# Kernel optimization log

Hardware: AMD Instinct MI355X
Metric: run time of the kernel (lower is better)

Reference implementation:

```python
import jax, jax.numpy as jnp
from jax import lax
import numpy as np

N, T, F, H, L, TOPK = 2048, 64, 16, 64, 16, 10


def setup_inputs() -> dict:
    key = jax.random.key(0)
    ks = jax.random.split(key, 12)
    s_ih = 1.0 / np.sqrt(H)
    inp = {
        "x": jax.random.normal(ks[0], (N, T, F), dtype=jnp.float32),
        # GRU params (torch layout: weight_ih_l0 (3H,F), weight_hh_l0 (3H,H))
        "W_ih": jax.random.uniform(ks[1], (3 * H, F), minval=-s_ih, maxval=s_ih),
        "W_hh": jax.random.uniform(ks[2], (3 * H, H), minval=-s_ih, maxval=s_ih),
        "b_ih": jax.random.uniform(ks[3], (3 * H,), minval=-s_ih, maxval=s_ih),
        "b_hh": jax.random.uniform(ks[4], (3 * H,), minval=-s_ih, maxval=s_ih),
        "Wq": jax.random.normal(ks[5], (H, H)) * (1.0 / np.sqrt(H)),
        "Wk": jax.random.normal(ks[6], (H, H)) * (1.0 / np.sqrt(H)),
        "W1": jax.random.normal(ks[7], (F, F)) * (1.0 / np.sqrt(F)),
        "b1": jnp.zeros((F,), jnp.float32),
        "W2": jax.random.normal(ks[8], (1, F)) * (1.0 / np.sqrt(F)),
        "b2": jnp.zeros((1,), jnp.float32),
    }
    return inp


def _gru(x, W_ih, W_hh, b_ih, b_hh):
    # x: (N, T, F) -> hidden states (N, T, H)
    xp = x @ W_ih.T + b_ih  # precompute input gates: (N, T, 3H)

    def step(h, xt):
        gh = h @ W_hh.T + b_hh
        xr, xz, xn = jnp.split(xt, 3, axis=-1)
        hr, hz, hn = jnp.split(gh, 3, axis=-1)
        r = jax.nn.sigmoid(xr + hr)
        z = jax.nn.sigmoid(xz + hz)
        n = jnp.tanh(xn + r * hn)
        h_new = (1.0 - z) * n + z * h
        return h_new, h_new

    h0 = jnp.zeros((x.shape[0], W_hh.shape[1]), x.dtype)
    _, hs = lax.scan(step, h0, jnp.swapaxes(xp, 0, 1))  # (T, N, H)
    return jnp.swapaxes(hs, 0, 1)


def reference(x, W_ih, W_hh, b_ih, b_hh, Wq, Wk, W1, b1, W2, b2):
    n, t, f = x.shape
    h = _gru(x, W_ih, W_hh, b_ih, b_hh)          # (N, T, H)
    queries = h[:, -1, :] @ Wq.T                 # (N, H)
    keys = h[:, -L:, :] @ Wk.T                   # (N, L, H)
    # cross-sample scores: query i vs key (stock m, lag l)
    scores = jnp.einsum("nh,mlh->nml", queries, keys)  # (N, N, L)
    eye = jnp.eye(n, dtype=bool)[:, :, None]
    scores = jnp.where(eye, jnp.float32(-1e9), scores)
    flat = scores.reshape(n, n * L)
    topk_vals, topk_idx = lax.top_k(flat, TOPK)  # order differs from torch sorted=False but math is permutation-invariant
    leader_idx = topk_idx // L                   # (N, k)
    lag_idx = topk_idx % L
    time_idx = t - (L - lag_idx)
    leader_feats = x[leader_idx, time_idx]       # (N, k, F)
    w = jax.nn.softmax(topk_vals, axis=1)
    weighted = jnp.sum(leader_feats * w[..., None], axis=1)  # (N, F)
    hid = jax.nn.leaky_relu(weighted @ W1.T + b1, negative_slope=0.01)
    out = (hid @ W2.T + b2).reshape(-1)          # (N,)
    return out
```

## Files before the change

### kernel.cpp

```cpp
#include <hip/hip_runtime.h>

#define NN 2048
#define TT 64
#define FF 16
#define HH 64
#define LL 16
#define TOPKK 10
#define CAP 960

#define AS 72
#define XAS 40
#define XPS 196

typedef __bf16 bf16x8 __attribute__((ext_vector_type(8)));
typedef float floatx4 __attribute__((ext_vector_type(4)));

union FragCast { uint4 u; bf16x8 b; unsigned short s[8]; };

__device__ __forceinline__ unsigned short f2bf(float f) {
    unsigned u = __float_as_uint(f);
    return (unsigned short)((u + 0x7fff + ((u >> 16) & 1)) >> 16);
}
__device__ __forceinline__ float bf2f(unsigned short h) {
    return __uint_as_float(((unsigned)h) << 16);
}
__device__ __forceinline__ void split3(float v, unsigned short& a, unsigned short& b, unsigned short& c) {
    a = f2bf(v); float r = v - bf2f(a);
    b = f2bf(r); float r2 = r - bf2f(b);
    c = f2bf(r2);
}
__device__ __forceinline__ float fsigmoid(float x) {
    return __builtin_amdgcn_rcpf(1.f + __builtin_amdgcn_exp2f(-1.442695041f * x));
}
__device__ __forceinline__ float ftanh(float x) {
    return 1.f - 2.f * __builtin_amdgcn_rcpf(1.f + __builtin_amdgcn_exp2f(2.885390082f * x));
}
__device__ __forceinline__ void async_copy16(const void* g, void* l) {
    __builtin_amdgcn_global_load_lds(
        (const __attribute__((address_space(1))) unsigned int*)g,
        (__attribute__((address_space(3))) unsigned int*)l, 16, 0, 0);
}
#define MFMA16(A, B, C) __builtin_amdgcn_mfma_f32_16x16x32_bf16((A), (B), (C), 0, 0, 0)
#define LIMB6(ACC, A1, A2, A3, W)            \
    ACC = MFMA16((A1), (W)[0], ACC);         \
    ACC = MFMA16((A1), (W)[1], ACC);         \
    ACC = MFMA16((A2), (W)[0], ACC);         \
    ACC = MFMA16((A1), (W)[2], ACC);         \
    ACC = MFMA16((A2), (W)[1], ACC);         \
    ACC = MFMA16((A3), (W)[0], ACC);

__global__ __launch_bounds__(256, 2) void gru_kernel(
    const float* __restrict__ x,
    const float* __restrict__ W_ih,
    const float* __restrict__ W_hh,
    const float* __restrict__ b_ih,
    const float* __restrict__ b_hh,
    float* __restrict__ h_tail)
{
    __shared__ __attribute__((aligned(16))) unsigned short Asp[2][3][16 * AS];
    __shared__ __attribute__((aligned(16))) unsigned short xa[3][16 * XAS];
    __shared__ __attribute__((aligned(16))) float xp[16 * XPS];
    __shared__ __attribute__((aligned(16))) float x_lds[4 * TT * FF];

    const int t    = threadIdx.x;
    const int wv   = t >> 6;
    const int lane = t & 63;
    const int nh   = lane & 15;
    const int quad = lane >> 4;
    const int n0   = blockIdx.x * 4;

    {
        const char* src = (const char*)(x + (size_t)n0 * TT * FF);
        char* dst = (char*)x_lds;
#pragma unroll
        for (int i = 0; i < 4; ++i)
            async_copy16(src + i * 4096 + t * 16, dst + i * 4096 + t * 16);
    }
    {
        unsigned* p = (unsigned*)&Asp[0][0][0];
        for (int i = t; i < 2 * 3 * 16 * AS / 2; i += 256) p[i] = 0;
        unsigned* q = (unsigned*)&xa[0][0];
        for (int i = t; i < 3 * 16 * XAS / 2; i += 256) q[i] = 0;
    }

    const int jb = wv * 16 + nh;
    const float brz = b_ih[jb] + b_hh[jb];
    const float bz  = b_ih[64 + jb] + b_hh[64 + jb];
    const float bxn = b_ih[128 + jb];
    const float bhn = b_hh[128 + jb];

    bf16x8 wf[3][2][3];
#pragma unroll
    for (int nt = 0; nt < 3; ++nt) {
        const int gr = (wv + 4 * nt) * 16 + nh;
#pragma unroll
        for (int kc = 0; kc < 2; ++kc) {
            const float* p = W_hh + gr * 64 + kc * 32 + quad * 8;
            FragCast f1, f2, f3;
#pragma unroll
            for (int i = 0; i < 8; ++i) split3(p[i], f1.s[i], f2.s[i], f3.s[i]);
            wf[nt][kc][0] = f1.b; wf[nt][kc][1] = f2.b; wf[nt][kc][2] = f3.b;
        }
    }
    bf16x8 wfi[3][3];
#pragma unroll
    for (int nt = 0; nt < 3; ++nt) {
        const int gr = (wv + 4 * nt) * 16 + nh;
        FragCast f1, f2, f3;
#pragma unroll
        for (int i = 0; i < 8; ++i) {
            const float v = (quad < 2) ? W_ih[gr * 16 + quad * 8 + i] : 0.f;
            split3(v, f1.s[i], f2.s[i], f3.s[i]);
        }
        wfi[nt][0] = f1.b; wfi[nt][1] = f2.b; wfi[nt][2] = f3.b;
    }

    __syncthreads();

    float hprev = 0.f;

    for (int chunk = 0; chunk < 16; ++chunk) {
        {
            const int row = t >> 4, f = t & 15;
            const int p = row & 3, sl = row >> 2;
            const float xv = x_lds[p * (TT * FF) + (chunk * 4 + sl) * FF + f];
            unsigned short a, b, c; split3(xv, a, b, c);
            xa[0][row * XAS + f] = a;
            xa[1][row * XAS + f] = b;
            xa[2][row * XAS + f] = c;
        }
        __syncthreads();
        {
            floatx4 xacc0 = {0.f,0.f,0.f,0.f}, xacc1 = {0.f,0.f,0.f,0.f}, xacc2 = {0.f,0.f,0.f,0.f};
            const int aoff = nh * XAS + quad * 8;
            FragCast a1, a2, a3;
            a1.u = *(const uint4*)&xa[0][aoff];
            a2.u = *(const uint4*)&xa[1][aoff];
            a3.u = *(const uint4*)&xa[2][aoff];
            LIMB6(xacc0, a1.b, a2.b, a3.b, wfi[0]);
            LIMB6(xacc1, a1.b, a2.b, a3.b, wfi[1]);
            LIMB6(xacc2, a1.b, a2.b, a3.b, wfi[2]);
#pragma unroll
            for (int r = 0; r < 4; ++r) {
                const int m = quad * 4 + r;
                xp[m * XPS + (wv + 0) * 16 + nh] = xacc0[r];
                xp[m * XPS + (wv + 4) * 16 + nh] = xacc1[r];
                xp[m * XPS + (wv + 8) * 16 + nh] = xacc2[r];
            }
        }
        __syncthreads();

#pragma unroll
        for (int si = 0; si < 4; ++si) {
            const int step = chunk * 4 + si;
            const int rb = step & 1, wb = rb ^ 1;
            floatx4 acc0 = {0.f,0.f,0.f,0.f}, acc1 = {0.f,0.f,0.f,0.f}, acc2 = {0.f,0.f,0.f,0.f};
#pragma unroll
            for (int kc = 0; kc < 2; ++kc) {
                const int aoff = nh * AS + kc * 32 + quad * 8;
                FragCast a1, a2, a3;
                a1.u = *(const uint4*)&Asp[rb][0][aoff];
                a2.u = *(const uint4*)&Asp[rb][1][aoff];
                a3.u = *(const uint4*)&Asp[rb][2][aoff];
                LIMB6(acc0, a1.b, a2.b, a3.b, wf[0][kc]);
                LIMB6(acc1, a1.b, a2.b, a3.b, wf[1][kc]);
                LIMB6(acc2, a1.b, a2.b, a3.b, wf[2][kc]);
            }
            {
                const int xrow = si * 4 + quad;
                const float xr = xp[xrow * XPS + jb];
                const float xz = xp[xrow * XPS + 64 + jb];
                const float xn = xp[xrow * XPS + 128 + jb];
                const float rg = fsigmoid(acc0[0] + xr + brz);
                const float zg = fsigmoid(acc1[0] + xz + bz);
                const float ng = ftanh((xn + bxn) + rg * (acc2[0] + bhn));
                const float h  = (1.f - zg) * ng + zg * hprev;
                hprev = h;
                unsigned short la, lb2, lc; split3(h, la, lb2, lc);
                const int ho = (4 * quad) * AS + jb;
                Asp[wb][0][ho] = la;
                Asp[wb][1][ho] = lb2;
                Asp[wb][2][ho] = lc;
                if (step >= TT - LL)
                    h_tail[((size_t)(n0 + quad) * LL + (step - (TT - LL))) * HH + jb] = h;
            }
            __syncthreads();
        }
    }
}

__global__ __launch_bounds__(256) void prep_kernel(
    const float* __restrict__ h_tail,
    const float* __restrict__ Wk,
    const float* __restrict__ Wq,
    float* __restrict__ Kmat,
    unsigned short* __restrict__ Kh,
    float* __restrict__ Qf,
    unsigned short* __restrict__ Qh)
{
    __shared__ __attribute__((aligned(16))) float Wk_s[64 * 68];
    __shared__ __attribute__((aligned(16))) float Wq_s[64 * 68];
    __shared__ __attribute__((aligned(16))) float hs2[16 * 68];
    const int t = threadIdx.x;
    const int n = blockIdx.x;

    for (int c = t; c < 1024; c += 256) {
        const int j = c >> 4, ci = c & 15;
        *(float4*)(Wk_s + j * 68 + ci * 4) = *(const float4*)(Wk + c * 4);
        *(float4*)(Wq_s + j * 68 + ci * 4) = *(const float4*)(Wq + c * 4);
    }
    {
        const int l = t >> 4, ci = t & 15;
        *(float4*)(hs2 + l * 68 + ci * 4) = *(const float4*)(h_tail + (size_t)n * 1024 + t * 4);
    }
    __syncthreads();

    const int l = t >> 4, qd = t & 15;
    float acc[4] = {0.f, 0.f, 0.f, 0.f};
#pragma unroll
    for (int ci = 0; ci < 16; ++ci) {
        const float4 hv = *(const float4*)(hs2 + l * 68 + ci * 4);
#pragma unroll
        for (int c = 0; c < 4; ++c) {
            const int j = qd + 16 * c;
            const float4 wv = *(const float4*)(Wk_s + j * 68 + ci * 4);
            acc[c] += hv.x * wv.x + hv.y * wv.y + hv.z * wv.z + hv.w * wv.w;
        }
    }
    const size_t row = (size_t)n * LL + l;
#pragma unroll
    for (int c = 0; c < 4; ++c) {
        const int col = qd + 16 * c;
        Kmat[row * 64 + col] = acc[c];
        Kh[row * 64 + col] = f2bf(acc[c]);
    }
    if (t < 64) {
        float a = 0.f;
#pragma unroll
        for (int i = 0; i < 64; ++i) a += hs2[15 * 68 + i] * Wq_s[t * 68 + i];
        Qf[(size_t)n * 64 + t] = a;
        Qh[(size_t)n * 64 + t] = f2bf(a);
    }
}

__global__ __launch_bounds__(512, 4) void score_kernel(
    const unsigned short* __restrict__ Kh,
    const unsigned short* __restrict__ Qh,
    int* __restrict__ cnt,
    int* __restrict__ ids)
{
    __shared__ float stat_s[8][4][16];
    __shared__ float stat_q[8][4][16];
    __shared__ float th_s[64];

    const int t    = threadIdx.x;
    const int wave = t >> 6;
    const int lane = t & 63;
    const int n    = lane & 15;
    const int quad = lane >> 4;

    const int qgroup = blockIdx.x >> 4;
    const int split  = blockIdx.x & 15;
    const int tile0  = split * 128 + wave * 16;

    FragCast bq[4][2];
#pragma unroll
    for (int qs = 0; qs < 4; ++qs) {
        const int qg = qgroup * 64 + qs * 16 + n;
        bq[qs][0].u = *(const uint4*)(Qh + (size_t)qg * 64 + quad * 8);
        bq[qs][1].u = *(const uint4*)(Qh + (size_t)qg * 64 + 32 + quad * 8);
    }

    float ssum[4] = {0.f,0.f,0.f,0.f}, ssq[4] = {0.f,0.f,0.f,0.f};
    for (int i = 0; i < 8; ++i) {
        const unsigned short* r = Kh + (size_t)((tile0 + i) * 16 + n) * 64;
        FragCast a0, a1;
        a0.u = *(const uint4*)(r + quad * 8);
        a1.u = *(const uint4*)(r + 32 + quad * 8);
#pragma unroll
        for (int qs = 0; qs < 4; ++qs) {
            floatx4 acc = {0.f, 0.f, 0.f, 0.f};
            acc = MFMA16(a0.b, bq[qs][0].b, acc);
            acc = MFMA16(a1.b, bq[qs][1].b, acc);
#pragma unroll
            for (int j = 0; j < 4; ++j) { ssum[qs] += acc[j]; ssq[qs] += acc[j] * acc[j]; }
        }
    }
#pragma unroll
    for (int qs = 0; qs < 4; ++qs) {
        ssum[qs] += __shfl_xor(ssum[qs], 16, 64); ssq[qs] += __shfl_xor(ssq[qs], 16, 64);
        ssum[qs] += __shfl_xor(ssum[qs], 32, 64); ssq[qs] += __shfl_xor(ssq[qs], 32, 64);
    }
    if (lane < 16) {
#pragma unroll
        for (int qs = 0; qs < 4; ++qs) { stat_s[wave][qs][n] = ssum[qs]; stat_q[wave][qs][n] = ssq[qs]; }
    }
    __syncthreads();
    if (t < 64) {
        const int qs = t >> 4, c = t & 15;
        float S = 0.f, S2 = 0.f;
#pragma unroll
        for (int w = 0; w < 8; ++w) { S += stat_s[w][qs][c]; S2 += stat_q[w][qs][c]; }
        const float inv = 1.f / 1024.f;
        const float mu = S * inv;
        float var = S2 * inv - mu * mu;
        var = var > 0.f ? var : 0.f;
        th_s[t] = mu + 2.6f * __fsqrt_rn(var);
    }
    __syncthreads();
    float th[4];
#pragma unroll
    for (int qs = 0; qs < 4; ++qs) th[qs] = th_s[qs * 16 + n];

    int bufp[16];
    int bcnt = 0;
    {
        FragCast a0, a1, na0, na1;
        const unsigned short* r0 = Kh + (size_t)(tile0 * 16 + n) * 64;
        a0.u = *(const uint4*)(r0 + quad * 8);
        a1.u = *(const uint4*)(r0 + 32 + quad * 8);
        for (int i = 0; i < 16; ++i) {
            if (i + 1 < 16) {
                const unsigned short* r = Kh + (size_t)((tile0 + i + 1) * 16 + n) * 64;
                na0.u = *(const uint4*)(r + quad * 8);
                na1.u = *(const uint4*)(r + 32 + quad * 8);
            }
            const int rowb = (tile0 + i) * 16 + quad * 4;
#pragma unroll
            for (int qs = 0; qs < 4; ++qs) {
                floatx4 acc = {0.f, 0.f, 0.f, 0.f};
                acc = MFMA16(a0.b, bq[qs][0].b, acc);
                acc = MFMA16(a1.b, bq[qs][1].b, acc);
                const int qg = qgroup * 64 + qs * 16 + n;
#pragma unroll
                for (int j = 0; j < 4; ++j) {
                    const float s = acc[j];
                    const int rowid = rowb + j;
                    if (s > th[qs] && (rowid >> 4) != qg && bcnt < 16) {
                        const int pk = qg * 32768 + rowid;
#pragma unroll
                        for (int k = 0; k < 16; ++k) if (k == bcnt) bufp[k] = pk;
                        bcnt++;
                    }
                }
            }
            a0 = na0; a1 = na1;
        }
    }
    if (bcnt > 0) {
#pragma unroll
        for (int k = 0; k < 16; ++k) {
            if (k < bcnt) {
                const int pk = bufp[k];
                const int qid = pk >> 15, rid = pk & 32767;
                const int slot = atomicAdd(&cnt[qid], 1);
                if (slot < CAP) ids[(size_t)qid * CAP + slot] = rid;
            }
        }
    }
}

__global__ __launch_bounds__(256) void final_kernel(
    const float* __restrict__ x,
    const float* __restrict__ Qf,
    const float* __restrict__ Kmat,
    const int* __restrict__ cnt,
    const int* __restrict__ ids,
    const float* __restrict__ W1, const float* __restrict__ b1,
    const float* __restrict__ W2, const float* __restrict__ b2,
    float* __restrict__ out)
{
    __shared__ __attribute__((aligned(16))) float Qs[8 * 64];
    __shared__ float sval[8][CAP];
    __shared__ int cnt_s[8];

    const int t = threadIdx.x;
    const int qbase = blockIdx.x * 8;

    if (t < 128) *(float4*)(Qs + t * 4) = *(const float4*)(Qf + (size_t)qbase * 64 + t * 4);
    if (t < 8) {
        int c = cnt[qbase + t];
        cnt_s[t] = c < CAP ? c : CAP;
    }
    __syncthreads();

    for (int q = 0; q < 8; ++q) {
        const int mc = cnt_s[q];
        const float* qr = Qs + q * 64;
        for (int c = t; c < mc; c += 256) {
            const int id = ids[(size_t)(qbase + q) * CAP + c];
            const float* kr = Kmat + (size_t)id * 64;
            float a0 = 0.f, a1 = 0.f, a2 = 0.f, a3 = 0.f;
#pragma unroll
            for (int i = 0; i < 64; i += 4) {
                a0 += qr[i] * kr[i];
                a1 += qr[i + 1] * kr[i + 1];
                a2 += qr[i + 2] * kr[i + 2];
                a3 += qr[i + 3] * kr[i + 3];
            }
            sval[q][c] = (a0 + a1) + (a2 + a3);
        }
    }
    __syncthreads();

    if (t < 8) {
        const int q = t, mc = cnt_s[q];
        float v[TOPKK]; int vid[TOPKK];
#pragma unroll
        for (int r = 0; r < TOPKK; ++r) { v[r] = -3e38f; vid[r] = -1; }
        float vmin = -3e38f; int imin = 0;
        for (int c = 0; c < mc; ++c) {
            const float s = sval[q][c];
            if (s > vmin) {
                const int id = ids[(size_t)(qbase + q) * CAP + c];
#pragma unroll
                for (int r = 0; r < TOPKK; ++r) if (r == imin) { v[r] = s; vid[r] = id; }
                vmin = v[0]; imin = 0;
#pragma unroll
                for (int r = 1; r < TOPKK; ++r) if (v[r] < vmin) { vmin = v[r]; imin = r; }
            }
        }
        float mx = v[0];
#pragma unroll
        for (int r = 1; r < TOPKK; ++r) mx = v[r] > mx ? v[r] : mx;
        float w[TOPKK]; float sum = 0.f;
#pragma unroll
        for (int r = 0; r < TOPKK; ++r) { w[r] = __expf(v[r] - mx); sum += w[r]; }
        const float inv = 1.f / sum;
        float feat[FF];
#pragma unroll
        for (int f = 0; f < FF; ++f) feat[f] = 0.f;
        for (int r = 0; r < TOPKK; ++r) {
            const int wi = vid[r];
            const int m = wi >> 4, l = wi & 15;
            const float* xr = x + ((size_t)m * TT + (48 + l)) * FF;
            const float wr = w[r] * inv;
#pragma unroll
            for (int f = 0; f < FF; ++f) feat[f] += wr * xr[f];
        }
        float o = 0.f;
#pragma unroll
        for (int oo = 0; oo < FF; ++oo) {
            float hh = b1[oo];
#pragma unroll
            for (int f = 0; f < FF; ++f) hh += feat[f] * W1[oo * FF + f];
            hh = hh > 0.f ? hh : 0.01f * hh;
            o += hh * W2[oo];
        }
        o += b2[0];
        out[qbase + t] = o;
    }
}

extern "C" void kernel_launch(void* const* d_in, const int* in_sizes, int n_in,
                              void* d_out, int out_size, void* d_ws, size_t ws_size,
                              hipStream_t stream) {
    const float* x    = (const float*)d_in[0];
    const float* W_ih = (const float*)d_in[1];
    const float* W_hh = (const float*)d_in[2];
    const float* b_ih = (const float*)d_in[3];
    const float* b_hh = (const float*)d_in[4];
    const float* Wq   = (const float*)d_in[5];
    const float* Wk   = (const float*)d_in[6];
    const float* W1   = (const float*)d_in[7];
    const float* b1   = (const float*)d_in[8];
    const float* W2   = (const float*)d_in[9];
    const float* b2   = (const float*)d_in[10];
    float* outp = (float*)d_out;
    (void)ws_size; (void)n_in; (void)in_sizes; (void)out_size;

    float* h_tail        = (float*)d_ws;
    int*   ids           = (int*)d_ws;
    float* Kmat          = h_tail + (size_t)2048 * 1024;
    unsigned short* Kh   = (unsigned short*)(Kmat + (size_t)32768 * 64);
    float* Qf            = (float*)(Kh + (size_t)32768 * 64);
    unsigned short* Qh   = (unsigned short*)(Qf + (size_t)2048 * 64);
    int*   cnt           = (int*)(Qh + (size_t)2048 * 64);

    hipMemsetAsync(cnt, 0, 2048 * sizeof(int), stream);
    gru_kernel<<<NN / 4, 256, 0, stream>>>(x, W_ih, W_hh, b_ih, b_hh, h_tail);
    prep_kernel<<<NN, 256, 0, stream>>>(h_tail, Wk, Wq, Kmat, Kh, Qf, Qh);
    score_kernel<<<512, 512, 0, stream>>>(Kh, Qh, cnt, ids);
    final_kernel<<<NN / 8, 256, 0, stream>>>(x, Qf, Kmat, cnt, ids, W1, b1, W2, b2, outp);
}
```

Baseline: 273.6 us.

## Fold cnt zeroing into GRU, register-tile prep kernel, and cooperative rescoring dot products

Zeroes the candidate counters inside the GRU kernel instead of a separate memset launch. The prep kernel drops its LDS staging and computes a 4x4 register tile per thread over 64 key rows per block, with 512 blocks instead of 2048. The Q projection is spread across all 256 threads. In the final kernel, each candidate's 64-wide dot product is now shared by 16 lanes using float4 loads and a shuffle reduction, giving coalesced Kmat reads. Weights are now read straight from global memory through the cache, not from LDS.

Result: slower. 336.0 us (+22.8%).

```diff
diff --git a/kernel.cpp b/kernel.cpp
--- a/kernel.cpp
+++ b/kernel.cpp
@@ -16,6 +16,7 @@
 typedef float floatx4 __attribute__((ext_vector_type(4)));
 
 union FragCast { uint4 u; bf16x8 b; unsigned short s[8]; };
+union Pack4 { unsigned short s[4]; uint2 u; };
 
 __device__ __forceinline__ unsigned short f2bf(float f) {
     unsigned u = __float_as_uint(f);
@@ -55,7 +56,8 @@
     const float* __restrict__ W_hh,
     const float* __restrict__ b_ih,
     const float* __restrict__ b_hh,
-    float* __restrict__ h_tail)
+    float* __restrict__ h_tail,
+    int* __restrict__ cnt)
 {
     __shared__ __attribute__((aligned(16))) unsigned short Asp[2][3][16 * AS];
     __shared__ __attribute__((aligned(16))) unsigned short xa[3][16 * XAS];
@@ -68,6 +70,8 @@
     const int nh   = lane & 15;
     const int quad = lane >> 4;
     const int n0   = blockIdx.x * 4;
+
+    if (t < 4) cnt[blockIdx.x * 4 + t] = 0;
 
     {
         const char* src = (const char*)(x + (size_t)n0 * TT * FF);
@@ -189,7 +193,7 @@
     }
 }
 
-__global__ __launch_bounds__(256) void prep_kernel(
+__global__ __launch_bounds__(256, 4) void prep_kernel(
     const float* __restrict__ h_tail,
     const float* __restrict__ Wk,
     const float* __restrict__ Wq,
@@ -198,48 +202,59 @@
     float* __restrict__ Qf,
     unsigned short* __restrict__ Qh)
 {
-    __shared__ __attribute__((aligned(16))) float Wk_s[64 * 68];
-    __shared__ __attribute__((aligned(16))) float Wq_s[64 * 68];
-    __shared__ __attribute__((aligned(16))) float hs2[16 * 68];
-    const int t = threadIdx.x;
-    const int n = blockIdx.x;
-
-    for (int c = t; c < 1024; c += 256) {
-        const int j = c >> 4, ci = c & 15;
-        *(float4*)(Wk_s + j * 68 + ci * 4) = *(const float4*)(Wk + c * 4);
-        *(float4*)(Wq_s + j * 68 + ci * 4) = *(const float4*)(Wq + c * 4);
-    }
+    const int t  = threadIdx.x;
+    const int rg = t >> 4;
+    const int cg = t & 15;
+    const size_t rbase = (size_t)blockIdx.x * 64;
+
+    float acc[4][4];
+#pragma unroll
+    for (int r = 0; r < 4; ++r)
+#pragma unroll
+        for (int c = 0; c < 4; ++c) acc[r][c] = 0.f;
+
+#pragma unroll
+    for (int ci = 0; ci < 16; ++ci) {
+        float4 hv[4], wv[4];
+#pragma unroll
+        for (int r = 0; r < 4; ++r)
+            hv[r] = *(const float4*)(h_tail + (rbase + rg * 4 + r) * 64 + ci * 4);
+#pragma unroll
+        for (int c = 0; c < 4; ++c)
+            wv[c] = *(const float4*)(Wk + (cg * 4 + c) * 64 + ci * 4);
+#pragma unroll
+        for (int r = 0; r < 4; ++r)
+#pragma unroll
+            for (int c = 0; c < 4; ++c)
+                acc[r][c] += hv[r].x * wv[c].x + hv[r].y * wv[c].y
+                           + hv[r].z * wv[c].z + hv[r].w * wv[c].w;
+    }
+#pragma unroll
+    for (int r = 0; r < 4; ++r) {
+        const size_t row = rbase + rg * 4 + r;
+        float4 o; o.x = acc[r][0]; o.y = acc[r][1]; o.z = acc[r][2]; o.w = acc[r][3];
+        *(float4*)(Kmat + row * 64 + cg * 4) = o;
+        Pack4 p;
+#pragma unroll
+        for (int c = 0; c < 4; ++c) p.s[c] = f2bf(acc[r][c]);
+        *(uint2*)(Kh + row * 64 + cg * 4) = p.u;
+    }
+
     {
-        const int l = t >> 4, ci = t & 15;
-        *(float4*)(hs2 + l * 68 + ci * 4) = *(const float4*)(h_tail + (size_t)n * 1024 + t * 4);
-    }
-    __syncthreads();
-
-    const int l = t >> 4, qd = t & 15;
-    float acc[4] = {0.f, 0.f, 0.f, 0.f};
-#pragma unroll
-    for (int ci = 0; ci < 16; ++ci) {
-        const float4 hv = *(const float4*)(hs2 + l * 68 + ci * 4);
-#pragma unroll
-        for (int c = 0; c < 4; ++c) {
-            const int j = qd + 16 * c;
-            const float4 wv = *(const float4*)(Wk_s + j * 68 + ci * 4);
-            acc[c] += hv.x * wv.x + hv.y * wv.y + hv.z * wv.z + hv.w * wv.w;
-        }
-    }
-    const size_t row = (size_t)n * LL + l;
-#pragma unroll
-    for (int c = 0; c < 4; ++c) {
-        const int col = qd + 16 * c;
-        Kmat[row * 64 + col] = acc[c];
-        Kh[row * 64 + col] = f2bf(acc[c]);
-    }
-    if (t < 64) {
-        float a = 0.f;
-#pragma unroll
-        for (int i = 0; i < 64; ++i) a += hs2[15 * 68 + i] * Wq_s[t * 68 + i];
-        Qf[(size_t)n * 64 + t] = a;
-        Qh[(size_t)n * 64 + t] = f2bf(a);
+        const int s = t >> 6, j = t & 63;
+        const float* hr = h_tail + ((size_t)(blockIdx.x * 4 + s) * LL + 15) * HH;
+        const float* wr = Wq + j * 64;
+        float a0 = 0.f, a1 = 0.f, a2 = 0.f, a3 = 0.f;
+#pragma unroll
+        for (int ci = 0; ci < 16; ++ci) {
+            const float4 h4 = *(const float4*)(hr + ci * 4);
+            const float4 w4 = *(const float4*)(wr + ci * 4);
+            a0 += h4.x * w4.x; a1 += h4.y * w4.y; a2 += h4.z * w4.z; a3 += h4.w * w4.w;
+        }
+        const float a = (a0 + a1) + (a2 + a3);
+        const size_t qi = (size_t)(blockIdx.x * 4 + s) * 64 + j;
+        Qf[qi] = a;
+        Qh[qi] = f2bf(a);
     }
 }
 
@@ -384,21 +399,22 @@
     }
     __syncthreads();
 
+    const int grp = t >> 4;
+    const int sl  = t & 15;
+
     for (int q = 0; q < 8; ++q) {
         const int mc = cnt_s[q];
-        const float* qr = Qs + q * 64;
-        for (int c = t; c < mc; c += 256) {
-            const int id = ids[(size_t)(qbase + q) * CAP + c];
-            const float* kr = Kmat + (size_t)id * 64;
-            float a0 = 0.f, a1 = 0.f, a2 = 0.f, a3 = 0.f;
-#pragma unroll
-            for (int i = 0; i < 64; i += 4) {
-                a0 += qr[i] * kr[i];
-                a1 += qr[i + 1] * kr[i + 1];
-                a2 += qr[i + 2] * kr[i + 2];
-                a3 += qr[i + 3] * kr[i + 3];
-            }
-            sval[q][c] = (a0 + a1) + (a2 + a3);
+        const float4 qv = *(const float4*)(Qs + q * 64 + sl * 4);
+        const int* idq = ids + (size_t)(qbase + q) * CAP;
+        for (int c = grp; c < mc; c += 16) {
+            const int id = idq[c];
+            const float4 kv = *(const float4*)(Kmat + (size_t)id * 64 + sl * 4);
+            float p = qv.x * kv.x + qv.y * kv.y + qv.z * kv.z + qv.w * kv.w;
+            p += __shfl_xor(p, 1, 64);
+            p += __shfl_xor(p, 2, 64);
+            p += __shfl_xor(p, 4, 64);
+            p += __shfl_xor(p, 8, 64);
+            if (sl == 0) sval[q][c] = p;
         }
     }
     __syncthreads();
@@ -477,9 +493,8 @@
     unsigned short* Qh   = (unsigned short*)(Qf + (size_t)2048 * 64);
     int*   cnt           = (int*)(Qh + (size_t)2048 * 64);
 
-    hipMemsetAsync(cnt, 0, 2048 * sizeof(int), stream);
-    gru_kernel<<<NN / 4, 256, 0, stream>>>(x, W_ih, W_hh, b_ih, b_hh, h_tail);
-    prep_kernel<<<NN, 256, 0, stream>>>(h_tail, Wk, Wq, Kmat, Kh, Qf, Qh);
+    gru_kernel<<<NN / 4, 256, 0, stream>>>(x, W_ih, W_hh, b_ih, b_hh, h_tail, cnt);
+    prep_kernel<<<512, 256, 0, stream>>>(h_tail, Wk, Wq, Kmat, Kh, Qf, Qh);
     score_kernel<<<512, 512, 0, stream>>>(Kh, Qh, cnt, ids);
     final_kernel<<<NN / 8, 256, 0, stream>>>(x, Qf, Kmat, cnt, ids, W1, b1, W2, b2, outp);
 }
```
